# Performance work log

Measured on AMD Instinct MI355X. Metric: run time of the kernel, lower is better.

Reference implementation:

```python
import jax, jax.numpy as jnp
import numpy as np

N = 65536        # collocation points
IN_DIM = 4       # x_dim=3 + is_unsteady=1
DEPTH = 256      # hidden width ('depth' arg)
HID = 5          # width-1 hidden tanh layers
OUT = 3


def setup_inputs() -> dict:
    key = jax.random.key(0)
    ks = jax.random.split(key, 4)
    def init(k, shape, fan_in):
        return jax.random.normal(k, shape, dtype=jnp.float32) / np.sqrt(fan_in).astype(np.float32)
    return {
        "x":  jax.random.normal(ks[0], (N, IN_DIM), dtype=jnp.float32),
        "W0": init(ks[1], (IN_DIM, DEPTH), IN_DIM),
        "b0": jnp.zeros((DEPTH,), jnp.float32),
        "Wh": init(ks[2], (HID, DEPTH, DEPTH), DEPTH),
        "bh": jnp.zeros((HID, DEPTH), jnp.float32),
        "Wl": init(ks[3], (DEPTH, OUT), DEPTH),
        "bl": jnp.zeros((OUT,), jnp.float32),
    }


def _mlp(x, W0, b0, Wh, bh, Wl, bl):
    # Faithful to nn.Sequential: first Linear has NO activation after it,
    # then (width-1) x [Linear, Tanh], then output Linear.
    h = x @ W0 + b0
    for i in range(HID):
        h = jnp.tanh(h @ Wh[i] + bh[i])
    return h @ Wl + bl  # vector potential a: [N, 3]


def reference(x, W0, b0, Wh, bh, Wl, bl):
    # curl(a) via 3 batched reverse-mode pulls (same math as torch autograd.grad
    # with grad_outputs = e_i repeated over the batch).
    a, vjp_fn = jax.vjp(lambda xx: _mlp(xx, W0, b0, Wh, bh, Wl, bl), x)
    e = jnp.eye(OUT, dtype=x.dtype)
    cots = jnp.broadcast_to(e[:, None, :], (OUT, x.shape[0], OUT))  # [3, N, 3]
    J = jax.vmap(lambda c: vjp_fn(c)[0])(cots)                      # [3, N, IN_DIM]
    da0dx, da1dx, da2dx = J[0], J[1], J[2]
    u = jnp.stack([
        da2dx[:, 1] - da1dx[:, 2],
        da0dx[:, 2] - da2dx[:, 0],
        da1dx[:, 0] - da0dx[:, 1],
    ], axis=1)  # [N, 3]
    return u
```

## Files before the change

### kernel.cpp

```cpp
#include <hip/hip_runtime.h>

typedef _Float16 f16;
typedef _Float16 f16x4 __attribute__((ext_vector_type(4)));
typedef _Float16 f16x8 __attribute__((ext_vector_type(8)));
typedef float    f32x4 __attribute__((ext_vector_type(4)));

#define OFF_WHP   0u
#define OFF_WLP   655360u
#define OFF_W0P   663552u
#define OFF_B0P   729088u
#define OFF_GP    745472u
#define OFF_BHP   794624u

__device__ __forceinline__ int phi(int kk, int g, int e){
  return (kk*2 + (e>>2))*16 + g*4 + (e&3);
}

__device__ __forceinline__ float tanh_fast(float z){
  float e = __builtin_amdgcn_exp2f(z * 2.885390081777927f);
  return 1.f - 2.f*__builtin_amdgcn_rcpf(e + 1.f);
}

__global__ void prepack(const float* __restrict__ W0, const float* __restrict__ b0,
                        const float* __restrict__ Wh, const float* __restrict__ bh,
                        const float* __restrict__ Wl, unsigned char* __restrict__ ws){
  int tid = blockIdx.x*256 + threadIdx.x;
  f16*   whp = (f16*)(ws + OFF_WHP);
  f16*   wlp = (f16*)(ws + OFF_WLP);
  float* w0p = (float*)(ws + OFF_W0P);
  float* b0p = (float*)(ws + OFF_B0P);
  float* gp  = (float*)(ws + OFF_GP);
  float* bhp = (float*)(ws + OFF_BHP);
  if (tid < 327680){
    int e=tid&7, lane=(tid>>3)&63, kk=(tid>>9)&7, nt=(tid>>12)&15, l=tid>>16;
    int k = phi(kk, lane>>4, e);
    int n = nt*16 + (lane&15);
    whp[tid] = (f16)Wh[(l*256 + k)*256 + n];
  } else if (tid < 331776){
    int t = tid - 327680;
    int e=t&7, lane=(t>>3)&63, kk=t>>9;
    int k = phi(kk, lane>>4, e);
    int n = lane&15;
    wlp[t] = (n<3) ? (f16)Wl[k*3+n] : (f16)0.f;
  } else if (tid < 335872){
    int t = tid - 331776;
    int e=t&7, lane=(t>>3)&63, kk=t>>9;
    int k = phi(kk, lane>>4, e);
    #pragma unroll
    for(int i=0;i<4;i++) w0p[t*4+i] = W0[i*256+k];
    b0p[t] = b0[k];
  } else if (tid < 348160){
    int t = tid - 335872;
    int e=t&7, lane=(t>>3)&63, kk=(t>>9)&7, j=t>>12;
    int k = phi(kk, lane>>4, e);
    float acc = 0.f;
    for(int k0=0;k0<256;k0++) acc = fmaf(W0[j*256+k0], Wh[k0*256+k], acc);
    gp[t] = acc;
  } else if (tid < 368640){
    int t = tid - 348160;
    int r=t&3, lane=(t>>2)&63, nt=(t>>8)&15, l=t>>12;
    bhp[t] = bh[l*256 + nt*16 + (lane>>4)*4 + r];
  }
}

__device__ __forceinline__ int moff(int lane, int kk){
  return lane*128 + ((kk ^ (lane & 7)) << 4);
}

__global__ __launch_bounds__(256, 2) void velcurl(
    const float* __restrict__ x, const unsigned char* __restrict__ ws,
    float* __restrict__ out){
  __shared__ __align__(16) char mbuf[2][2][8192];
  __shared__ float outt[2][3][3][16];

  const int lane  = threadIdx.x & 63;
  const int w     = threadIdx.x >> 6;
  const int s     = lane & 15;
  const int sbase = blockIdx.x << 5;

  const f16x8* __restrict__ whp = (const f16x8*)(ws + OFF_WHP);
  const f16x8* __restrict__ wlp = (const f16x8*)(ws + OFF_WLP);
  const f32x4* __restrict__ w0p = (const f32x4*)(ws + OFF_W0P);
  const float* __restrict__ b0p = (const float*)(ws + OFF_B0P);
  const float* __restrict__ gp  = (const float*)(ws + OFF_GP);
  const f32x4* __restrict__ bhp = (const f32x4*)(ws + OFF_BHP);

  f16x8 st[2][8];
  f16x8 nst[2][8];

  if (w==0){
    const f32x4 xv0 = ((const f32x4*)x)[sbase + s];
    const f32x4 xv1 = ((const f32x4*)x)[sbase + 16 + s];
    #pragma unroll
    for(int kk=0;kk<8;kk++){
      f16x8 v0, v1;
      #pragma unroll
      for(int e=0;e<8;e++){
        f32x4 wv = w0p[(kk*64+lane)*8+e];
        float b  = b0p[(kk*64+lane)*8+e];
        v0[e] = (f16)fmaf(xv0[3],wv[3], fmaf(xv0[2],wv[2], fmaf(xv0[1],wv[1], fmaf(xv0[0],wv[0], b))));
        v1[e] = (f16)fmaf(xv1[3],wv[3], fmaf(xv1[2],wv[2], fmaf(xv1[1],wv[1], fmaf(xv1[0],wv[0], b))));
      }
      st[0][kk] = v0; st[1][kk] = v1;
    }
    f16x8 mc0, mc1;
    #pragma unroll
    for(int nt=0;nt<16;nt++){
      f32x4 a0 = {0.f,0.f,0.f,0.f}, a1 = {0.f,0.f,0.f,0.f};
      #pragma unroll
      for(int kk=0;kk<8;kk++){
        f16x8 frag = whp[(nt*8+kk)*64+lane];
        a0 = __builtin_amdgcn_mfma_f32_16x16x32_f16(frag, st[0][kk], a0, 0,0,0);
        a1 = __builtin_amdgcn_mfma_f32_16x16x32_f16(frag, st[1][kk], a1, 0,0,0);
      }
      f32x4 bv = bhp[nt*64+lane];
      #pragma unroll
      for(int r=0;r<4;r++){
        float h0 = tanh_fast(a0[r]+bv[r]);
        float h1 = tanh_fast(a1[r]+bv[r]);
        nst[0][nt>>1][(nt&1)*4+r] = (f16)h0;
        nst[1][nt>>1][(nt&1)*4+r] = (f16)h1;
        mc0[(nt&1)*4+r] = (f16)(1.f - h0*h0);
        mc1[(nt&1)*4+r] = (f16)(1.f - h1*h1);
      }
      if (nt&1){
        *(f16x8*)(&mbuf[0][0][0] + moff(lane, nt>>1)) = mc0;
        *(f16x8*)(&mbuf[0][1][0] + moff(lane, nt>>1)) = mc1;
      }
    }
    #pragma unroll
    for(int kk=0;kk<8;kk++){ st[0][kk]=nst[0][kk]; st[1][kk]=nst[1][kk]; }
  }
  __syncthreads();

  #pragma unroll 1
  for(int p=1;p<5;p++){
    const f16x8* wl = whp + p*8192;
    if (w==0){
      const f32x4* bp = bhp + p*1024;
      f16x8 mc0, mc1;
      #pragma unroll
      for(int nt=0;nt<16;nt++){
        f32x4 a0 = {0.f,0.f,0.f,0.f}, a1 = {0.f,0.f,0.f,0.f};
        #pragma unroll
        for(int kk=0;kk<8;kk++){
          f16x8 frag = wl[(nt*8+kk)*64+lane];
          a0 = __builtin_amdgcn_mfma_f32_16x16x32_f16(frag, st[0][kk], a0, 0,0,0);
          a1 = __builtin_amdgcn_mfma_f32_16x16x32_f16(frag, st[1][kk], a1, 0,0,0);
        }
        f32x4 bv = bp[nt*64+lane];
        #pragma unroll
        for(int r=0;r<4;r++){
          float h0 = tanh_fast(a0[r]+bv[r]);
          float h1 = tanh_fast(a1[r]+bv[r]);
          nst[0][nt>>1][(nt&1)*4+r] = (f16)h0;
          nst[1][nt>>1][(nt&1)*4+r] = (f16)h1;
          mc0[(nt&1)*4+r] = (f16)(1.f - h0*h0);
          mc1[(nt&1)*4+r] = (f16)(1.f - h1*h1);
        }
        if (nt&1){
          *(f16x8*)(&mbuf[p&1][0][0] + moff(lane, nt>>1)) = mc0;
          *(f16x8*)(&mbuf[p&1][1][0] + moff(lane, nt>>1)) = mc1;
        }
      }
      #pragma unroll
      for(int kk=0;kk<8;kk++){ st[0][kk]=nst[0][kk]; st[1][kk]=nst[1][kk]; }
    } else {
      const char* mb0 = &mbuf[(p-1)&1][0][0];
      const char* mb1 = &mbuf[(p-1)&1][1][0];
      if (p==1){
        const int j = w-1;
        #pragma unroll
        for(int kk=0;kk<8;kk++){
          f16x8 m80 = *(const f16x8*)(mb0 + moff(lane, kk));
          f16x8 m81 = *(const f16x8*)(mb1 + moff(lane, kk));
          f16x8 v0, v1;
          #pragma unroll
          for(int e=0;e<8;e++){
            float gv = gp[((j*8+kk)*64+lane)*8 + e];
            v0[e] = (f16)((float)m80[e] * gv);
            v1[e] = (f16)((float)m81[e] * gv);
          }
          st[0][kk] = v0; st[1][kk] = v1;
        }
      } else {
        #pragma unroll
        for(int kk=0;kk<8;kk++){
          f16x8 m80 = *(const f16x8*)(mb0 + moff(lane, kk));
          f16x8 m81 = *(const f16x8*)(mb1 + moff(lane, kk));
          st[0][kk] = m80 * nst[0][kk];
          st[1][kk] = m81 * nst[1][kk];
        }
      }
      #pragma unroll
      for(int nt=0;nt<16;nt++){
        f32x4 a0 = {0.f,0.f,0.f,0.f}, a1 = {0.f,0.f,0.f,0.f};
        #pragma unroll
        for(int kk=0;kk<8;kk++){
          f16x8 frag = wl[(nt*8+kk)*64+lane];
          a0 = __builtin_amdgcn_mfma_f32_16x16x32_f16(frag, st[0][kk], a0, 0,0,0);
          a1 = __builtin_amdgcn_mfma_f32_16x16x32_f16(frag, st[1][kk], a1, 0,0,0);
        }
        #pragma unroll
        for(int r=0;r<4;r++){
          nst[0][nt>>1][(nt&1)*4+r] = (f16)a0[r];
          nst[1][nt>>1][(nt&1)*4+r] = (f16)a1[r];
        }
      }
    }
    __syncthreads();
  }

  if (w>0){
    const char* mb0 = &mbuf[0][0][0];
    const char* mb1 = &mbuf[0][1][0];
    f32x4 a0 = {0.f,0.f,0.f,0.f}, a1 = {0.f,0.f,0.f,0.f};
    #pragma unroll
    for(int kk=0;kk<8;kk++){
      f16x8 frag = wlp[kk*64+lane];
      f16x8 m80 = *(const f16x8*)(mb0 + moff(lane, kk));
      f16x8 m81 = *(const f16x8*)(mb1 + moff(lane, kk));
      a0 = __builtin_amdgcn_mfma_f32_16x16x32_f16(frag, m80 * nst[0][kk], a0, 0,0,0);
      a1 = __builtin_amdgcn_mfma_f32_16x16x32_f16(frag, m81 * nst[1][kk], a1, 0,0,0);
    }
    if (lane<16){
      outt[0][w-1][0][lane] = a0[0];
      outt[0][w-1][1][lane] = a0[1];
      outt[0][w-1][2][lane] = a0[2];
      outt[1][w-1][0][lane] = a1[0];
      outt[1][w-1][1][lane] = a1[1];
      outt[1][w-1][2][lane] = a1[2];
    }
  }
  __syncthreads();

  if (w==0 && lane<32){
    const int t = lane>>4, ss = lane&15;
    const int so = (sbase + lane)*3;
    out[so+0] = outt[t][1][2][ss] - outt[t][2][1][ss];
    out[so+1] = outt[t][2][0][ss] - outt[t][0][2][ss];
    out[so+2] = outt[t][0][1][ss] - outt[t][1][0][ss];
  }
}

extern "C" void kernel_launch(void* const* d_in, const int* in_sizes, int n_in,
                              void* d_out, int out_size, void* d_ws, size_t ws_size,
                              hipStream_t stream){
  const float* x  = (const float*)d_in[0];
  const float* W0 = (const float*)d_in[1];
  const float* b0 = (const float*)d_in[2];
  const float* Wh = (const float*)d_in[3];
  const float* bh = (const float*)d_in[4];
  const float* Wl = (const float*)d_in[5];
  prepack<<<1440, 256, 0, stream>>>(W0, b0, Wh, bh, Wl, (unsigned char*)d_ws);
  velcurl<<<2048, 256, 0, stream>>>(x, (const unsigned char*)d_ws, (float*)d_out);
}
```

Measured before the change: 381.3 us.

## Stage hidden-layer weight tiles into LDS cooperatively with async global_load_lds double buffering

Each block now copies every hidden layer's weight fragments into a double-buffered LDS tile using global_load_lds, split across all four waves, instead of each wave reading weights from global memory on its own. Each layer is processed in eight 2-column-tile chunks, with the next chunk prefetched while the current one is consumed. The separate first-layer prologue is folded into the loop, and the gp loads are vectorised. This shares weight traffic across the forward and tangent waves, at the cost of two barriers per chunk and 32KB more LDS, which may lower occupancy.

After: 376.5 us. Within noise of the previous version (-1.2%).

```diff
diff --git a/kernel.cpp b/kernel.cpp
--- a/kernel.cpp
+++ b/kernel.cpp
@@ -1,7 +1,6 @@
 #include <hip/hip_runtime.h>
 
 typedef _Float16 f16;
-typedef _Float16 f16x4 __attribute__((ext_vector_type(4)));
 typedef _Float16 f16x8 __attribute__((ext_vector_type(8)));
 typedef float    f32x4 __attribute__((ext_vector_type(4)));
 
@@ -67,9 +66,21 @@
   return lane*128 + ((kk ^ (lane & 7)) << 4);
 }
 
+__device__ __forceinline__ void gload16(const void* g, void* l){
+  __builtin_amdgcn_global_load_lds(
+      (const __attribute__((address_space(1))) void*)g,
+      (__attribute__((address_space(3))) void*)l, 16, 0, 0);
+}
+#define VMW4() asm volatile("s_waitcnt vmcnt(4)" ::: "memory")
+#define VMW0() asm volatile("s_waitcnt vmcnt(0)" ::: "memory")
+#define LGK0() asm volatile("s_waitcnt lgkmcnt(0)" ::: "memory")
+#define BARRIER() do{ asm volatile("" ::: "memory"); __builtin_amdgcn_s_barrier(); \
+                      asm volatile("" ::: "memory"); }while(0)
+
 __global__ __launch_bounds__(256, 2) void velcurl(
     const float* __restrict__ x, const unsigned char* __restrict__ ws,
     float* __restrict__ out){
+  __shared__ __align__(16) char wbuf[2][16384];
   __shared__ __align__(16) char mbuf[2][2][8192];
   __shared__ float outt[2][3][3][16];
 
@@ -88,81 +99,31 @@
   f16x8 st[2][8];
   f16x8 nst[2][8];
 
-  if (w==0){
-    const f32x4 xv0 = ((const f32x4*)x)[sbase + s];
-    const f32x4 xv1 = ((const f32x4*)x)[sbase + 16 + s];
-    #pragma unroll
-    for(int kk=0;kk<8;kk++){
-      f16x8 v0, v1;
-      #pragma unroll
-      for(int e=0;e<8;e++){
-        f32x4 wv = w0p[(kk*64+lane)*8+e];
-        float b  = b0p[(kk*64+lane)*8+e];
-        v0[e] = (f16)fmaf(xv0[3],wv[3], fmaf(xv0[2],wv[2], fmaf(xv0[1],wv[1], fmaf(xv0[0],wv[0], b))));
-        v1[e] = (f16)fmaf(xv1[3],wv[3], fmaf(xv1[2],wv[2], fmaf(xv1[1],wv[1], fmaf(xv1[0],wv[0], b))));
-      }
-      st[0][kk] = v0; st[1][kk] = v1;
-    }
-    f16x8 mc0, mc1;
-    #pragma unroll
-    for(int nt=0;nt<16;nt++){
-      f32x4 a0 = {0.f,0.f,0.f,0.f}, a1 = {0.f,0.f,0.f,0.f};
-      #pragma unroll
-      for(int kk=0;kk<8;kk++){
-        f16x8 frag = whp[(nt*8+kk)*64+lane];
-        a0 = __builtin_amdgcn_mfma_f32_16x16x32_f16(frag, st[0][kk], a0, 0,0,0);
-        a1 = __builtin_amdgcn_mfma_f32_16x16x32_f16(frag, st[1][kk], a1, 0,0,0);
-      }
-      f32x4 bv = bhp[nt*64+lane];
-      #pragma unroll
-      for(int r=0;r<4;r++){
-        float h0 = tanh_fast(a0[r]+bv[r]);
-        float h1 = tanh_fast(a1[r]+bv[r]);
-        nst[0][nt>>1][(nt&1)*4+r] = (f16)h0;
-        nst[1][nt>>1][(nt&1)*4+r] = (f16)h1;
-        mc0[(nt&1)*4+r] = (f16)(1.f - h0*h0);
-        mc1[(nt&1)*4+r] = (f16)(1.f - h1*h1);
-      }
-      if (nt&1){
-        *(f16x8*)(&mbuf[0][0][0] + moff(lane, nt>>1)) = mc0;
-        *(f16x8*)(&mbuf[0][1][0] + moff(lane, nt>>1)) = mc1;
-      }
-    }
-    #pragma unroll
-    for(int kk=0;kk<8;kk++){ st[0][kk]=nst[0][kk]; st[1][kk]=nst[1][kk]; }
-  }
-  __syncthreads();
-
   #pragma unroll 1
-  for(int p=1;p<5;p++){
+  for(int p=0;p<5;p++){
     const f16x8* wl = whp + p*8192;
-    if (w==0){
-      const f32x4* bp = bhp + p*1024;
-      f16x8 mc0, mc1;
-      #pragma unroll
-      for(int nt=0;nt<16;nt++){
-        f32x4 a0 = {0.f,0.f,0.f,0.f}, a1 = {0.f,0.f,0.f,0.f};
+    #pragma unroll
+    for(int i=0;i<4;i++)
+      gload16((const void*)(wl + (w*4+i)*64 + lane), (void*)(&wbuf[0][0] + (w*4+i)*1024));
+
+    if (p==0){
+      if (w==0){
+        const f32x4 xv0 = ((const f32x4*)x)[sbase + s];
+        const f32x4 xv1 = ((const f32x4*)x)[sbase + 16 + s];
         #pragma unroll
         for(int kk=0;kk<8;kk++){
-          f16x8 frag = wl[(nt*8+kk)*64+lane];
-          a0 = __builtin_amdgcn_mfma_f32_16x16x32_f16(frag, st[0][kk], a0, 0,0,0);
-          a1 = __builtin_amdgcn_mfma_f32_16x16x32_f16(frag, st[1][kk], a1, 0,0,0);
-        }
-        f32x4 bv = bp[nt*64+lane];
-        #pragma unroll
-        for(int r=0;r<4;r++){
-          float h0 = tanh_fast(a0[r]+bv[r]);
-          float h1 = tanh_fast(a1[r]+bv[r]);
-          nst[0][nt>>1][(nt&1)*4+r] = (f16)h0;
-          nst[1][nt>>1][(nt&1)*4+r] = (f16)h1;
-          mc0[(nt&1)*4+r] = (f16)(1.f - h0*h0);
-          mc1[(nt&1)*4+r] = (f16)(1.f - h1*h1);
-        }
-        if (nt&1){
-          *(f16x8*)(&mbuf[p&1][0][0] + moff(lane, nt>>1)) = mc0;
-          *(f16x8*)(&mbuf[p&1][1][0] + moff(lane, nt>>1)) = mc1;
-        }
-      }
+          f16x8 v0, v1;
+          #pragma unroll
+          for(int e=0;e<8;e++){
+            f32x4 wv = w0p[(kk*64+lane)*8+e];
+            float b  = b0p[(kk*64+lane)*8+e];
+            v0[e] = (f16)fmaf(xv0[3],wv[3], fmaf(xv0[2],wv[2], fmaf(xv0[1],wv[1], fmaf(xv0[0],wv[0], b))));
+            v1[e] = (f16)fmaf(xv1[3],wv[3], fmaf(xv1[2],wv[2], fmaf(xv1[1],wv[1], fmaf(xv1[0],wv[0], b))));
+          }
+          st[0][kk] = v0; st[1][kk] = v1;
+        }
+      }
+    } else if (w==0){
       #pragma unroll
       for(int kk=0;kk<8;kk++){ st[0][kk]=nst[0][kk]; st[1][kk]=nst[1][kk]; }
     } else {
@@ -170,14 +131,17 @@
       const char* mb1 = &mbuf[(p-1)&1][1][0];
       if (p==1){
         const int j = w-1;
+        const f32x4* gpv = (const f32x4*)gp;
         #pragma unroll
         for(int kk=0;kk<8;kk++){
           f16x8 m80 = *(const f16x8*)(mb0 + moff(lane, kk));
           f16x8 m81 = *(const f16x8*)(mb1 + moff(lane, kk));
+          f32x4 g0 = gpv[((j*8+kk)*64+lane)*2+0];
+          f32x4 g1 = gpv[((j*8+kk)*64+lane)*2+1];
           f16x8 v0, v1;
           #pragma unroll
           for(int e=0;e<8;e++){
-            float gv = gp[((j*8+kk)*64+lane)*8 + e];
+            float gv = (e<4) ? g0[e&3] : g1[e&3];
             v0[e] = (f16)((float)m80[e] * gv);
             v1[e] = (f16)((float)m81[e] * gv);
           }
@@ -192,23 +156,70 @@
           st[1][kk] = m81 * nst[1][kk];
         }
       }
-      #pragma unroll
-      for(int nt=0;nt<16;nt++){
-        f32x4 a0 = {0.f,0.f,0.f,0.f}, a1 = {0.f,0.f,0.f,0.f};
-        #pragma unroll
-        for(int kk=0;kk<8;kk++){
-          f16x8 frag = wl[(nt*8+kk)*64+lane];
-          a0 = __builtin_amdgcn_mfma_f32_16x16x32_f16(frag, st[0][kk], a0, 0,0,0);
-          a1 = __builtin_amdgcn_mfma_f32_16x16x32_f16(frag, st[1][kk], a1, 0,0,0);
-        }
-        #pragma unroll
-        for(int r=0;r<4;r++){
-          nst[0][nt>>1][(nt&1)*4+r] = (f16)a0[r];
-          nst[1][nt>>1][(nt&1)*4+r] = (f16)a1[r];
-        }
-      }
-    }
-    __syncthreads();
+    }
+
+    #pragma unroll
+    for(int e=0;e<8;e++){
+      if (e<7){
+        char* dst = &wbuf[(e+1)&1][0];
+        #pragma unroll
+        for(int i=0;i<4;i++)
+          gload16((const void*)(wl + ((e+1)*16 + w*4+i)*64 + lane),
+                  (void*)(dst + (w*4+i)*1024));
+        VMW4();
+      } else {
+        VMW0();
+      }
+      BARRIER();
+      const f16x8* wb = (const f16x8*)&wbuf[e&1][0];
+      if (w==0){
+        const f32x4* bp = bhp + p*1024;
+        f16x8 mc0, mc1;
+        #pragma unroll
+        for(int d=0;d<2;d++){
+          const int nt = 2*e+d;
+          f32x4 a0 = {0.f,0.f,0.f,0.f}, a1 = {0.f,0.f,0.f,0.f};
+          #pragma unroll
+          for(int kk=0;kk<8;kk++){
+            f16x8 frag = wb[(d*8+kk)*64+lane];
+            a0 = __builtin_amdgcn_mfma_f32_16x16x32_f16(frag, st[0][kk], a0, 0,0,0);
+            a1 = __builtin_amdgcn_mfma_f32_16x16x32_f16(frag, st[1][kk], a1, 0,0,0);
+          }
+          f32x4 bv = bp[nt*64+lane];
+          #pragma unroll
+          for(int r=0;r<4;r++){
+            float h0 = tanh_fast(a0[r]+bv[r]);
+            float h1 = tanh_fast(a1[r]+bv[r]);
+            nst[0][e][d*4+r] = (f16)h0;
+            nst[1][e][d*4+r] = (f16)h1;
+            mc0[d*4+r] = (f16)(1.f - h0*h0);
+            mc1[d*4+r] = (f16)(1.f - h1*h1);
+          }
+          if (d==1){
+            *(f16x8*)(&mbuf[p&1][0][0] + moff(lane, e)) = mc0;
+            *(f16x8*)(&mbuf[p&1][1][0] + moff(lane, e)) = mc1;
+          }
+        }
+      } else if (p>=1){
+        #pragma unroll
+        for(int d=0;d<2;d++){
+          f32x4 a0 = {0.f,0.f,0.f,0.f}, a1 = {0.f,0.f,0.f,0.f};
+          #pragma unroll
+          for(int kk=0;kk<8;kk++){
+            f16x8 frag = wb[(d*8+kk)*64+lane];
+            a0 = __builtin_amdgcn_mfma_f32_16x16x32_f16(frag, st[0][kk], a0, 0,0,0);
+            a1 = __builtin_amdgcn_mfma_f32_16x16x32_f16(frag, st[1][kk], a1, 0,0,0);
+          }
+          #pragma unroll
+          for(int r=0;r<4;r++){
+            nst[0][e][d*4+r] = (f16)a0[r];
+            nst[1][e][d*4+r] = (f16)a1[r];
+          }
+        }
+      }
+      LGK0();
+      BARRIER();
+    }
   }
 
   if (w>0){
@@ -232,7 +243,8 @@
       outt[1][w-1][2][lane] = a1[2];
     }
   }
-  __syncthreads();
+  LGK0();
+  BARRIER();
 
   if (w==0 && lane<32){
     const int t = lane>>4, ss = lane&15;
```
